# Kernel tuning notes

Hardware: AMD Instinct MI355X
Metric: run time of the kernel (lower is better)

Reference implementation:

```python
import jax, jax.numpy as jnp
import numpy as np

EPS_BN = 1e-5
EPS_ATTN = 1e-9


def bn(h, g, b, m, v):
    # inference-mode BatchNorm1d over channel (last) dim
    return (h - m) * (g * jax.lax.rsqrt(v + EPS_BN)) + b


def setup_inputs() -> dict:
    key = jax.random.key(0)
    ks = jax.random.split(key, 16)
    B, N, Cin, C = 16, 2048, 64, 256
    std = 0.05
    inp = {
        "x": jax.random.normal(ks[0], (B, N, Cin), jnp.float32),
        "w1": jax.random.normal(ks[1], (C, Cin), jnp.float32) * std,
        "w2": jax.random.normal(ks[2], (C, C), jnp.float32) * std,
        "wqk": jax.random.normal(ks[3], (C, C), jnp.float32) * std,
        "wv": jax.random.normal(ks[4], (C, C), jnp.float32) * std,
        "bv": jax.random.normal(ks[5], (C,), jnp.float32) * std,
        "wt": jax.random.normal(ks[6], (C, C), jnp.float32) * std,
        "bt": jax.random.normal(ks[7], (C,), jnp.float32) * std,
    }
    for i, name in enumerate(["bn1", "bn2", "bn3"]):
        k = jax.random.split(ks[8 + i], 4)
        inp[name + "_g"] = 1.0 + 0.1 * jax.random.normal(k[0], (C,), jnp.float32)
        inp[name + "_b"] = 0.1 * jax.random.normal(k[1], (C,), jnp.float32)
        inp[name + "_m"] = 0.1 * jax.random.normal(k[2], (C,), jnp.float32)
        inp[name + "_v"] = jax.random.uniform(k[3], (C,), jnp.float32, 0.5, 1.5)
    return inp


def reference(x, w1, w2, wqk, wv, bv, wt, bt,
              bn1_g, bn1_b, bn1_m, bn1_v,
              bn2_g, bn2_b, bn2_m, bn2_v,
              bn3_g, bn3_b, bn3_m, bn3_v):
    # x: [B, N, Cin]; all feature maps kept channel-last [B, N, C]
    h = jax.nn.relu(bn(jnp.einsum('bnc,dc->bnd', x, w1), bn1_g, bn1_b, bn1_m, bn1_v))
    h = jax.nn.relu(bn(jnp.einsum('bnc,dc->bnd', h, w2), bn2_g, bn2_b, bn2_m, bn2_v))

    # SA_Layer: q and k share the same (bias-free) 1x1 conv weights
    q = jnp.einsum('bnc,dc->bnd', h, wqk)          # [B,N,C]
    energy = jnp.einsum('bic,bjc->bij', q, q)      # [B,N,N]
    attn = jax.nn.softmax(energy, axis=-1)
    attn = attn / (EPS_ATTN + jnp.sum(attn, axis=1, keepdims=True))  # L1 renorm over queries
    v = jnp.einsum('bnc,dc->bnd', h, wv) + bv      # [B,N,C]
    x_r = jnp.einsum('bic,bij->bjc', v, attn)      # [B,N,C]

    t = jnp.einsum('bnc,dc->bnd', h - x_r, wt) + bt
    t = jax.nn.relu(bn(t, bn3_g, bn3_b, bn3_m, bn3_v))
    out = h + t                                    # [B,N,C]
    return jnp.transpose(out, (0, 2, 1))           # [B,C,N] as in torch module
```

## Files before the change

kernel.cpp:

```cpp
#include <hip/hip_runtime.h>
#include <hip/hip_bf16.h>

#define B_  16
#define N_  2048
#define C_  256
#define BN_ (B_*N_)

typedef __bf16 bf16x8 __attribute__((ext_vector_type(8)));
typedef float  f32x4  __attribute__((ext_vector_type(4)));
typedef int    i32x4  __attribute__((ext_vector_type(4)));

static __device__ __forceinline__ f32x4 MFMA(bf16x8 a, bf16x8 b, f32x4 c){
  return __builtin_amdgcn_mfma_f32_16x16x32_bf16(a, b, c, 0, 0, 0);
}
static __device__ __forceinline__ unsigned short f2b(float f){
  unsigned int u = __float_as_uint(f);
  u += 0x7fffu + ((u >> 16) & 1u);
  return (unsigned short)(u >> 16);
}

__global__ void prep_kernel(
    const float* __restrict__ w1, const float* __restrict__ w2,
    const float* __restrict__ wqk, const float* __restrict__ wv,
    const float* __restrict__ bv, const float* __restrict__ wt,
    const float* __restrict__ bt,
    const float* __restrict__ g1, const float* __restrict__ b1,
    const float* __restrict__ m1, const float* __restrict__ v1,
    const float* __restrict__ g2, const float* __restrict__ b2,
    const float* __restrict__ m2, const float* __restrict__ v2,
    const float* __restrict__ g3, const float* __restrict__ b3,
    const float* __restrict__ m3, const float* __restrict__ v3,
    unsigned short* __restrict__ w1b, unsigned short* __restrict__ w2b,
    unsigned short* __restrict__ wqkb, unsigned short* __restrict__ wvb,
    unsigned short* __restrict__ wtb,
    float* __restrict__ bias1, float* __restrict__ bias2,
    float* __restrict__ biasv, float* __restrict__ biast)
{
  const int d = blockIdx.x;
  const int c = threadIdx.x;
  const float s1 = g1[d] * rsqrtf(v1[d] + 1e-5f);
  const float s2 = g2[d] * rsqrtf(v2[d] + 1e-5f);
  const float s3 = g3[d] * rsqrtf(v3[d] + 1e-5f);
  if (c < 64) w1b[d*64 + c] = f2b(w1[d*64 + c] * s1);
  w2b[d*256 + c]  = f2b(w2[d*256 + c] * s2);
  wqkb[d*256 + c] = f2b(wqk[d*256 + c]);
  wvb[d*256 + c]  = f2b(wv[d*256 + c]);
  wtb[d*256 + c]  = f2b(wt[d*256 + c] * s3);
  if (c == 0){
    bias1[d] = b1[d] - m1[d]*s1;
    bias2[d] = b2[d] - m2[d]*s2;
    biasv[d] = bv[d];
    biast[d] = bt[d]*s3 + b3[d] - m3[d]*s3;
  }
}

template<int MODE, int K>
__global__ __launch_bounds__(256, 2) void wgemm(
    const void* __restrict__ inp, const unsigned short* __restrict__ wB,
    const float* __restrict__ bias, const float* __restrict__ hf32,
    void* __restrict__ out0, void* __restrict__ out1)
{
  extern __shared__ char smem[];
  unsigned short* Al = (unsigned short*)smem;
  unsigned short* Bl = (unsigned short*)(smem + 64*72*2);
  const int tid  = threadIdx.x;
  const int lane = tid & 63;
  const int w    = tid >> 6;
  const int wr   = w >> 1, wc = w & 1;
  const long row0 = (long)blockIdx.x * 64;

  f32x4 acc[2][8];
  #pragma unroll
  for (int m = 0; m < 2; ++m)
    #pragma unroll
    for (int n = 0; n < 8; ++n) acc[m][n] = f32x4{0.f,0.f,0.f,0.f};

  const int KS = K / 64;
  #pragma unroll 1
  for (int s = 0; s < KS; ++s){
    if (s) __syncthreads();
    if constexpr (MODE == 0){
      const float* xin = (const float*)inp;
      #pragma unroll
      for (int t = 0; t < 4; ++t){
        int idx = tid + t*256;
        int r = idx >> 4, c4 = (idx & 15) * 4;
        float4 v = *(const float4*)(xin + (row0 + r)*K + c4);
        unsigned short* dst = &Al[r*72 + c4];
        dst[0]=f2b(v.x); dst[1]=f2b(v.y); dst[2]=f2b(v.z); dst[3]=f2b(v.w);
      }
    } else {
      const unsigned short* bin = (const unsigned short*)inp;
      #pragma unroll
      for (int t = 0; t < 2; ++t){
        int idx = tid + t*256;
        int r = idx >> 3, c8 = (idx & 7) * 8;
        *(i32x4*)&Al[r*72 + c8] = *(const i32x4*)(bin + (row0 + r)*K + s*64 + c8);
      }
    }
    #pragma unroll
    for (int t = 0; t < 8; ++t){
      int idx = tid + t*256;
      int d = idx >> 3, c8 = (idx & 7) * 8;
      *(i32x4*)&Bl[d*72 + c8] = *(const i32x4*)(wB + d*K + s*64 + c8);
    }
    __syncthreads();
    #pragma unroll
    for (int kk = 0; kk < 2; ++kk){
      bf16x8 a[2], b[8];
      #pragma unroll
      for (int m = 0; m < 2; ++m)
        a[m] = *(const bf16x8*)&Al[(32*wr + 16*m + (lane&15))*72 + kk*32 + (lane>>4)*8];
      #pragma unroll
      for (int n = 0; n < 8; ++n)
        b[n] = *(const bf16x8*)&Bl[(128*wc + 16*n + (lane&15))*72 + kk*32 + (lane>>4)*8];
      #pragma unroll
      for (int m = 0; m < 2; ++m)
        #pragma unroll
        for (int n = 0; n < 8; ++n)
          acc[m][n] = MFMA(a[m], b[n], acc[m][n]);
    }
  }

  if constexpr (MODE <= 2){
    unsigned short* obf = (unsigned short*)out0;
    float* of = (float*)out1;
    float sq[2][4];
    #pragma unroll
    for (int m = 0; m < 2; ++m)
      #pragma unroll
      for (int r = 0; r < 4; ++r) sq[m][r] = 0.f;
    #pragma unroll
    for (int n = 0; n < 8; ++n){
      int col = 128*wc + 16*n + (lane&15);
      float bs = 0.f;
      if constexpr (MODE != 2) bs = bias[col];
      #pragma unroll
      for (int m = 0; m < 2; ++m){
        int rl = 32*wr + 16*m + (lane>>4)*4;
        #pragma unroll
        for (int r = 0; r < 4; ++r){
          float v = acc[m][n][r] + bs;
          if constexpr (MODE == 0 || MODE == 1) v = fmaxf(v, 0.f);
          obf[(row0 + rl + r)*256 + col] = f2b(v);
          if constexpr (MODE == 1) of[(row0 + rl + r)*256 + col] = v;
          if constexpr (MODE == 2) sq[m][r] += v*v;
        }
      }
    }
    if constexpr (MODE == 2){
      #pragma unroll
      for (int m = 0; m < 2; ++m)
        #pragma unroll
        for (int r = 0; r < 4; ++r){
          float s = sq[m][r];
          s += __shfl_xor(s, 1); s += __shfl_xor(s, 2);
          s += __shfl_xor(s, 4); s += __shfl_xor(s, 8);
          sq[m][r] = s;
        }
      __syncthreads();
      float* ssq = (float*)smem;
      if (tid < 64) ssq[tid] = 0.f;
      __syncthreads();
      if ((lane & 15) == 0){
        #pragma unroll
        for (int m = 0; m < 2; ++m)
          #pragma unroll
          for (int r = 0; r < 4; ++r)
            atomicAdd(&ssq[32*wr + 16*m + (lane>>4)*4 + r], sq[m][r]);
      }
      __syncthreads();
      if (tid < 64) ((float*)out1)[row0 + tid] = ssq[tid];
    }
  } else if constexpr (MODE == 3){
    __syncthreads();
    unsigned short* Vl = (unsigned short*)smem;
    #pragma unroll
    for (int n = 0; n < 8; ++n){
      int col = 128*wc + 16*n + (lane&15);
      float bs = bias[col];
      #pragma unroll
      for (int m = 0; m < 2; ++m){
        int rl = 32*wr + 16*m + (lane>>4)*4;
        #pragma unroll
        for (int r = 0; r < 4; ++r)
          Vl[(rl + r)*264 + col] = f2b(acc[m][n][r] + bs);
      }
    }
    __syncthreads();
    long b = row0 >> 11;
    int  n0 = (int)(row0 & 2047);
    unsigned short* vt = (unsigned short*)out0 + b*(256L*2048);
    #pragma unroll 1
    for (int cc = 0; cc < 64; ++cc){
      int c = 64*w + cc;
      vt[(long)c*2048 + n0 + lane] = Vl[lane*264 + c];
    }
  } else {
    __syncthreads();
    float* Ol = (float*)smem;
    #pragma unroll
    for (int n = 0; n < 8; ++n){
      int col = 128*wc + 16*n + (lane&15);
      float bs = bias[col];
      #pragma unroll
      for (int m = 0; m < 2; ++m){
        int rl = 32*wr + 16*m + (lane>>4)*4;
        #pragma unroll
        for (int r = 0; r < 4; ++r){
          float t = fmaxf(acc[m][n][r] + bs, 0.f);
          float h = hf32[(row0 + rl + r)*256 + col];
          Ol[(rl + r)*265 + col] = h + t;
        }
      }
    }
    __syncthreads();
    long b = row0 >> 11;
    int  n0 = (int)(row0 & 2047);
    float* op = (float*)out0 + b*(256L*2048);
    #pragma unroll 1
    for (int cc = 0; cc < 64; ++cc){
      int c = 64*w + cc;
      op[(long)c*2048 + n0 + lane] = Ol[lane*265 + c];
    }
  }
}

__global__ __launch_bounds__(256, 2) void pass1_kernel(
    const unsigned short* __restrict__ q,
    const float* __restrict__ rowm, float* __restrict__ rowl)
{
  __shared__ unsigned short qi[64*264];
  __shared__ float sll[4][64];
  const int tid = threadIdx.x, lane = tid & 63, w = tid >> 6;
  const int l15 = lane & 15, hi = lane >> 4;
  const int lin = blockIdx.y * 32 + blockIdx.x;
  const int swz = (lin & 7) * 64 + (lin >> 3);
  const int b  = swz >> 5;
  const int i0 = (swz & 31) * 64;
  const unsigned short* qb = q + (long)b*N_*C_;

  #pragma unroll
  for (int t = 0; t < 8; ++t){
    int idx = tid + t*256;
    int r = idx >> 5, c8 = (idx & 31) * 8;
    *(i32x4*)&qi[r*264 + c8] = *(const i32x4*)(qb + (long)(i0 + r)*256 + c8);
  }

  float mi[4], lacc[4];
  #pragma unroll
  for (int ii = 0; ii < 4; ++ii){
    mi[ii] = rowm[(long)b*N_ + i0 + 16*ii + l15];
    lacc[ii] = 0.f;
  }
  __syncthreads();

  #pragma unroll 1
  for (int js = 0; js < 8; ++js){
    const int j0 = js*256 + 64*w;
    #pragma unroll
    for (int h = 0; h < 2; ++h){
      f32x4 e[2][4];
      #pragma unroll
      for (int jf = 0; jf < 2; ++jf)
        #pragma unroll
        for (int ii = 0; ii < 4; ++ii) e[jf][ii] = f32x4{0.f,0.f,0.f,0.f};

      #pragma unroll 1
      for (int kk = 0; kk < 8; ++kk){
        bf16x8 aa[4], bb[2];
        #pragma unroll
        for (int ii = 0; ii < 4; ++ii)
          aa[ii] = *(const bf16x8*)&qi[(16*ii + l15)*264 + kk*32 + hi*8];
        #pragma unroll
        for (int jf = 0; jf < 2; ++jf)
          bb[jf] = *(const bf16x8*)(qb + (long)(j0 + 16*(2*h + jf) + l15)*256 + kk*32 + hi*8);
        #pragma unroll
        for (int jf = 0; jf < 2; ++jf)
          #pragma unroll
          for (int ii = 0; ii < 4; ++ii)
            e[jf][ii] = MFMA(bb[jf], aa[ii], e[jf][ii]);
      }

      #pragma unroll
      for (int ii = 0; ii < 4; ++ii){
        float p = 0.f;
        #pragma unroll
        for (int jf = 0; jf < 2; ++jf)
          #pragma unroll
          for (int r = 0; r < 4; ++r)
            p += __expf(e[jf][ii][r] - mi[ii]);
        lacc[ii] += p;
      }
    }
  }

  #pragma unroll
  for (int ii = 0; ii < 4; ++ii){
    float l0 = lacc[ii];
    l0 += __shfl_xor(l0, 16);
    l0 += __shfl_xor(l0, 32);
    if (lane < 16) sll[w][16*ii + l15] = l0;
  }
  __syncthreads();
  if (tid < 64)
    rowl[(long)b*N_ + i0 + tid] = sll[0][tid] + sll[1][tid] + sll[2][tid] + sll[3][tid];
}

__global__ __launch_bounds__(256, 2) void pass2_kernel(
    const unsigned short* __restrict__ q, const unsigned short* __restrict__ vT,
    const float* __restrict__ rowm, const float* __restrict__ rowl,
    const float* __restrict__ hf, unsigned short* __restrict__ dbf)
{
  extern __shared__ char smem[];
  unsigned short* qj = (unsigned short*)smem;
  unsigned short* pl = qj + 64*264;
  float* colsum = (float*)(pl + 64*264);
  const int tid = threadIdx.x, lane = tid & 63, w = tid >> 6;
  const int lin = blockIdx.y * 32 + blockIdx.x;
  const int swz = (lin & 7) * 64 + (lin >> 3);
  const int b  = swz >> 5;
  const int j0 = (swz & 31) * 64;
  const unsigned short* qb = q  + (long)b*N_*C_;
  const unsigned short* vb = vT + (long)b*N_*C_;
  const float* mrow = rowm + (long)b*N_;
  const float* lrow = rowl + (long)b*N_;

  #pragma unroll
  for (int t = 0; t < 8; ++t){
    int idx = tid + t*256;
    int r = idx >> 5, c8 = (idx & 31) * 8;
    *(i32x4*)&qj[r*264 + c8] = *(const i32x4*)(qb + (long)(j0 + r)*256 + c8);
  }
  if (tid < 64) colsum[tid] = 0.f;
  __syncthreads();

  float cs[4][4];
  #pragma unroll
  for (int a = 0; a < 4; ++a)
    #pragma unroll
    for (int r = 0; r < 4; ++r) cs[a][r] = 0.f;
  f32x4 nm[4][4];
  #pragma unroll
  for (int a = 0; a < 4; ++a)
    #pragma unroll
    for (int c = 0; c < 4; ++c) nm[a][c] = f32x4{0.f,0.f,0.f,0.f};

  unsigned int pk[4][4][2];

  #pragma unroll 1
  for (int is = 0; is < 8; ++is){
    const int i0 = is * 256;
    const int iw = i0 + 64*w;

    float mi[4], ri[4];
    #pragma unroll
    for (int f = 0; f < 4; ++f){
      int ig = iw + 16*f + (lane&15);
      mi[f] = mrow[ig];
      ri[f] = __builtin_amdgcn_rcpf(lrow[ig]);
    }

    f32x4 e[4][4];
    #pragma unroll
    for (int a = 0; a < 4; ++a)
      #pragma unroll
      for (int f = 0; f < 4; ++f) e[a][f] = f32x4{0.f,0.f,0.f,0.f};
    #pragma unroll
    for (int kk = 0; kk < 8; ++kk){
      bf16x8 a[4], bb[4];
      #pragma unroll
      for (int jf = 0; jf < 4; ++jf)
        a[jf] = *(const bf16x8*)&qj[(16*jf + (lane&15))*264 + kk*32 + (lane>>4)*8];
      #pragma unroll
      for (int f = 0; f < 4; ++f)
        bb[f] = *(const bf16x8*)(qb + (long)(iw + 16*f + (lane&15))*256 + kk*32 + (lane>>4)*8);
      #pragma unroll
      for (int jf = 0; jf < 4; ++jf)
        #pragma unroll
        for (int f = 0; f < 4; ++f)
          e[jf][f] = MFMA(a[jf], bb[f], e[jf][f]);
    }

    if (is > 0){
      const int ip = i0 - 256;
      #pragma unroll
      for (int kc = 0; kc < 8; ++kc){
        bf16x8 pa[4], vv[4];
        #pragma unroll
        for (int jf = 0; jf < 4; ++jf)
          pa[jf] = *(const bf16x8*)&pl[(16*jf + (lane&15))*264 + kc*32 + (lane>>4)*8];
        #pragma unroll
        for (int cf = 0; cf < 4; ++cf)
          vv[cf] = *(const bf16x8*)(vb + (long)(64*w + 16*cf + (lane&15))*2048 + ip + kc*32 + (lane>>4)*8);
        #pragma unroll
        for (int jf = 0; jf < 4; ++jf)
          #pragma unroll
          for (int cf = 0; cf < 4; ++cf)
            nm[jf][cf] = MFMA(pa[jf], vv[cf], nm[jf][cf]);
      }
    }

    #pragma unroll
    for (int f = 0; f < 4; ++f){
      #pragma unroll
      for (int jf = 0; jf < 4; ++jf){
        #pragma unroll
        for (int rp = 0; rp < 2; ++rp){
          float p0 = __expf(e[jf][f][2*rp]   - mi[f]) * ri[f];
          float p1 = __expf(e[jf][f][2*rp+1] - mi[f]) * ri[f];
          cs[jf][2*rp]   += p0;
          cs[jf][2*rp+1] += p1;
          pk[jf][f][rp] = (unsigned int)f2b(p0) | ((unsigned int)f2b(p1) << 16);
        }
      }
    }

    __syncthreads();
    #pragma unroll
    for (int jf = 0; jf < 4; ++jf)
      #pragma unroll
      for (int f = 0; f < 4; ++f)
        #pragma unroll
        for (int rp = 0; rp < 2; ++rp){
          unsigned int v = pk[jf][f][rp];
          int col = 64*w + 16*f + (lane&15);
          pl[(16*jf + (lane>>4)*4 + 2*rp)*264 + col]     = (unsigned short)v;
          pl[(16*jf + (lane>>4)*4 + 2*rp+1)*264 + col]   = (unsigned short)(v >> 16);
        }
    __syncthreads();
  }

  {
    const int ip = 7 * 256;
    #pragma unroll
    for (int kc = 0; kc < 8; ++kc){
      bf16x8 pa[4], vv[4];
      #pragma unroll
      for (int jf = 0; jf < 4; ++jf)
        pa[jf] = *(const bf16x8*)&pl[(16*jf + (lane&15))*264 + kc*32 + (lane>>4)*8];
      #pragma unroll
      for (int cf = 0; cf < 4; ++cf)
        vv[cf] = *(const bf16x8*)(vb + (long)(64*w + 16*cf + (lane&15))*2048 + ip + kc*32 + (lane>>4)*8);
      #pragma unroll
      for (int jf = 0; jf < 4; ++jf)
        #pragma unroll
        for (int cf = 0; cf < 4; ++cf)
          nm[jf][cf] = MFMA(pa[jf], vv[cf], nm[jf][cf]);
    }
  }

  #pragma unroll
  for (int jf = 0; jf < 4; ++jf)
    #pragma unroll
    for (int r = 0; r < 4; ++r){
      float v = cs[jf][r];
      v += __shfl_xor(v, 1); v += __shfl_xor(v, 2);
      v += __shfl_xor(v, 4); v += __shfl_xor(v, 8);
      if ((lane & 15) == 0) atomicAdd(&colsum[16*jf + (lane>>4)*4 + r], v);
    }
  __syncthreads();

  #pragma unroll
  for (int jf = 0; jf < 4; ++jf)
    #pragma unroll
    for (int r = 0; r < 4; ++r){
      int jl = 16*jf + (lane>>4)*4 + r;
      float rcs = __builtin_amdgcn_rcpf(1e-9f + colsum[jl]);
      long rowg = (long)b*N_ + j0 + jl;
      #pragma unroll
      for (int cf = 0; cf < 4; ++cf){
        int c = 64*w + 16*cf + (lane&15);
        float xr = nm[jf][cf][r] * rcs;
        float d = hf[rowg*256 + c] - xr;
        dbf[rowg*256 + c] = f2b(d);
      }
    }
}

extern "C" void kernel_launch(void* const* d_in, const int* in_sizes, int n_in,
                              void* d_out, int out_size, void* d_ws, size_t ws_size,
                              hipStream_t stream)
{
  const float* x   = (const float*)d_in[0];
  const float* w1  = (const float*)d_in[1];
  const float* w2  = (const float*)d_in[2];
  const float* wqk = (const float*)d_in[3];
  const float* wv  = (const float*)d_in[4];
  const float* bv  = (const float*)d_in[5];
  const float* wt  = (const float*)d_in[6];
  const float* bt  = (const float*)d_in[7];
  const float* g1 = (const float*)d_in[8],  *b1 = (const float*)d_in[9];
  const float* m1 = (const float*)d_in[10], *v1 = (const float*)d_in[11];
  const float* g2 = (const float*)d_in[12], *b2 = (const float*)d_in[13];
  const float* m2 = (const float*)d_in[14], *v2 = (const float*)d_in[15];
  const float* g3 = (const float*)d_in[16], *b3 = (const float*)d_in[17];
  const float* m3 = (const float*)d_in[18], *v3 = (const float*)d_in[19];

  char* ws = (char*)d_ws;
  size_t off = 0;
  auto alloc = [&](size_t bytes)->char*{
    char* p = ws + off; off += (bytes + 255) & ~(size_t)255; return p;
  };
  unsigned short* w1b  = (unsigned short*)alloc(256*64*2);
  unsigned short* w2b  = (unsigned short*)alloc(256*256*2);
  unsigned short* wqkb = (unsigned short*)alloc(256*256*2);
  unsigned short* wvb  = (unsigned short*)alloc(256*256*2);
  unsigned short* wtb  = (unsigned short*)alloc(256*256*2);
  float* bias1 = (float*)alloc(256*4);
  float* bias2 = (float*)alloc(256*4);
  float* biasv = (float*)alloc(256*4);
  float* biast = (float*)alloc(256*4);
  unsigned short* h1_bf = (unsigned short*)alloc((size_t)BN_*C_*2);
  float*          h_f32 = (float*)alloc((size_t)BN_*C_*4);
  unsigned short* h_bf  = (unsigned short*)alloc((size_t)BN_*C_*2);
  unsigned short* q_bf  = (unsigned short*)alloc((size_t)BN_*C_*2);
  unsigned short* vT_bf = (unsigned short*)alloc((size_t)BN_*C_*2);
  float* rowm = (float*)alloc((size_t)BN_*4);
  float* rowl = (float*)alloc((size_t)BN_*4);
  unsigned short* d_bf  = (unsigned short*)alloc((size_t)BN_*C_*2);
  (void)ws_size; (void)in_sizes; (void)n_in; (void)out_size;

  hipFuncSetAttribute((const void*)&pass2_kernel,
                      hipFuncAttributeMaxDynamicSharedMemorySize, 67840);
  hipFuncSetAttribute((const void*)&wgemm<4,256>,
                      hipFuncAttributeMaxDynamicSharedMemorySize, 67840);

  prep_kernel<<<256, 256, 0, stream>>>(w1, w2, wqk, wv, bv, wt, bt,
      g1,b1,m1,v1, g2,b2,m2,v2, g3,b3,m3,v3,
      w1b, w2b, wqkb, wvb, wtb, bias1, bias2, biasv, biast);

  wgemm<0,64><<<512, 256, 46080, stream>>>(x, w1b, bias1, nullptr, h1_bf, nullptr);
  wgemm<1,256><<<512, 256, 46080, stream>>>(h1_bf, w2b, bias2, nullptr, h_bf, h_f32);
  wgemm<2,256><<<512, 256, 46080, stream>>>(h_bf, wqkb, nullptr, nullptr, q_bf, rowm);
  wgemm<3,256><<<512, 256, 46080, stream>>>(h_bf, wvb, biasv, nullptr, vT_bf, nullptr);

  pass1_kernel<<<dim3(32,16), 256, 0, stream>>>(q_bf, rowm, rowl);
  pass2_kernel<<<dim3(32,16), 256, 67840, stream>>>(q_bf, vT_bf, rowm, rowl, h_f32, d_bf);

  wgemm<4,256><<<512, 256, 67840, stream>>>(d_bf, wtb, biast, h_f32, d_out, nullptr);
}
```

Before: 360.7 us.

## Restructure pass1 with register-resident query tiles and double-buffered swizzled LDS key staging

pass1 now keeps each wave's 16 query rows in registers and streams 32-row key tiles into a double-buffered, XOR-swizzled shared-memory buffer. Where the builtin is available it uses global_load_lds, so the next tile loads while the current one is computed. Before, every wave read its key rows straight from global memory and the query tile sat in LDS. The launch bound rises to 4 blocks per CU to raise occupancy. The cost is a barrier on every one of 64 iterations and only two MFMAs per k-step per wave, which lowers compute intensity per loaded byte.

```diff
diff --git a/kernel.cpp b/kernel.cpp
--- a/kernel.cpp
+++ b/kernel.cpp
@@ -226,12 +226,11 @@
   }
 }
 
-__global__ __launch_bounds__(256, 2) void pass1_kernel(
+__global__ __launch_bounds__(256, 4) void pass1_kernel(
     const unsigned short* __restrict__ q,
     const float* __restrict__ rowm, float* __restrict__ rowl)
 {
-  __shared__ unsigned short qi[64*264];
-  __shared__ float sll[4][64];
+  __shared__ unsigned short jbuf[2][32*256];
   const int tid = threadIdx.x, lane = tid & 63, w = tid >> 6;
   const int l15 = lane & 15, hi = lane >> 4;
   const int lin = blockIdx.y * 32 + blockIdx.x;
@@ -240,71 +239,64 @@
   const int i0 = (swz & 31) * 64;
   const unsigned short* qb = q + (long)b*N_*C_;
 
-  #pragma unroll
-  for (int t = 0; t < 8; ++t){
-    int idx = tid + t*256;
-    int r = idx >> 5, c8 = (idx & 31) * 8;
-    *(i32x4*)&qi[r*264 + c8] = *(const i32x4*)(qb + (long)(i0 + r)*256 + c8);
-  }
-
-  float mi[4], lacc[4];
-  #pragma unroll
-  for (int ii = 0; ii < 4; ++ii){
-    mi[ii] = rowm[(long)b*N_ + i0 + 16*ii + l15];
-    lacc[ii] = 0.f;
-  }
+  bf16x8 bqi[8];
+  #pragma unroll
+  for (int kk = 0; kk < 8; ++kk)
+    bqi[kk] = *(const bf16x8*)(qb + (long)(i0 + 16*w + l15)*256 + kk*32 + hi*8);
+  const float mi = rowm[(long)b*N_ + i0 + 16*w + l15];
+  float lacc = 0.f;
+
+  const char* qbb = (const char*)qb;
+
+  auto stage = [&](int sel, int js){
+    const char* src = qbb + (size_t)js * (32*512);
+    #pragma unroll
+    for (int t = 0; t < 4; ++t){
+      int idx = t*256 + tid;
+      int row = idx >> 5, c16 = idx & 31;
+      const char* g = src + (size_t)row*512 + ((c16*16) ^ ((row & 7) << 4));
+#if __has_builtin(__builtin_amdgcn_global_load_lds)
+      char* l = (char*)&jbuf[sel][0] + (size_t)(t*256 + w*64)*16;
+      __builtin_amdgcn_global_load_lds(
+          (const __attribute__((address_space(1))) void*)g,
+          (__attribute__((address_space(3))) void*)l, 16, 0, 0);
+#else
+      *(i32x4*)((char*)&jbuf[sel][0] + (size_t)idx*16) = *(const i32x4*)g;
+#endif
+    }
+  };
+
+  stage(0, 0);
   __syncthreads();
 
   #pragma unroll 1
-  for (int js = 0; js < 8; ++js){
-    const int j0 = js*256 + 64*w;
-    #pragma unroll
-    for (int h = 0; h < 2; ++h){
-      f32x4 e[2][4];
-      #pragma unroll
-      for (int jf = 0; jf < 2; ++jf)
-        #pragma unroll
-        for (int ii = 0; ii < 4; ++ii) e[jf][ii] = f32x4{0.f,0.f,0.f,0.f};
-
-      #pragma unroll 1
-      for (int kk = 0; kk < 8; ++kk){
-        bf16x8 aa[4], bb[2];
-        #pragma unroll
-        for (int ii = 0; ii < 4; ++ii)
-          aa[ii] = *(const bf16x8*)&qi[(16*ii + l15)*264 + kk*32 + hi*8];
-        #pragma unroll
-        for (int jf = 0; jf < 2; ++jf)
-          bb[jf] = *(const bf16x8*)(qb + (long)(j0 + 16*(2*h + jf) + l15)*256 + kk*32 + hi*8);
-        #pragma unroll
-        for (int jf = 0; jf < 2; ++jf)
-          #pragma unroll
-          for (int ii = 0; ii < 4; ++ii)
-            e[jf][ii] = MFMA(bb[jf], aa[ii], e[jf][ii]);
-      }
-
-      #pragma unroll
-      for (int ii = 0; ii < 4; ++ii){
-        float p = 0.f;
-        #pragma unroll
-        for (int jf = 0; jf < 2; ++jf)
-          #pragma unroll
-          for (int r = 0; r < 4; ++r)
-            p += __expf(e[jf][ii][r] - mi[ii]);
-        lacc[ii] += p;
-      }
-    }
-  }
-
-  #pragma unroll
-  for (int ii = 0; ii < 4; ++ii){
-    float l0 = lacc[ii];
-    l0 += __shfl_xor(l0, 16);
-    l0 += __shfl_xor(l0, 32);
-    if (lane < 16) sll[w][16*ii + l15] = l0;
-  }
-  __syncthreads();
-  if (tid < 64)
-    rowl[(long)b*N_ + i0 + tid] = sll[0][tid] + sll[1][tid] + sll[2][tid] + sll[3][tid];
+  for (int js = 0; js < 64; ++js){
+    const int cur = js & 1;
+    if (js < 63) stage(cur ^ 1, js + 1);
+
+    const char* jb = (const char*)&jbuf[cur][0];
+    const int sx = (l15 & 7) << 4;
+    f32x4 e0 = f32x4{0.f,0.f,0.f,0.f};
+    f32x4 e1 = f32x4{0.f,0.f,0.f,0.f};
+    #pragma unroll
+    for (int kk = 0; kk < 8; ++kk){
+      int colb = kk*64 + hi*16;
+      bf16x8 a0 = *(const bf16x8*)(jb + (size_t)l15*512        + (colb ^ sx));
+      bf16x8 a1 = *(const bf16x8*)(jb + (size_t)(16+l15)*512   + (colb ^ sx));
+      e0 = MFMA(a0, bqi[kk], e0);
+      e1 = MFMA(a1, bqi[kk], e1);
+    }
+    float p = __expf(e0[0]-mi) + __expf(e0[1]-mi) + __expf(e0[2]-mi) + __expf(e0[3]-mi)
+            + __expf(e1[0]-mi) + __expf(e1[1]-mi) + __expf(e1[2]-mi) + __expf(e1[3]-mi);
+    lacc += p;
+
+    __syncthreads();
+  }
+
+  lacc += __shfl_xor(lacc, 16);
+  lacc += __shfl_xor(lacc, 32);
+  if (lane < 16)
+    rowl[(long)b*N_ + i0 + 16*w + l15] = lacc;
 }
 
 __global__ __launch_bounds__(256, 2) void pass2_kernel(
```

Result: faster. 348.0 us (-3.5%).
